# Performance work log

Hardware: AMD Instinct MI355X
Metric: run time of the kernel (lower is better)

The kernel has to match this reference:

```python
import jax, jax.numpy as jnp
import numpy as np

D_MODEL = 1024
N_HEADS = 16
HEAD_DIM = D_MODEL // N_HEADS


def setup_inputs() -> dict:
    key = jax.random.key(0)
    ks = jax.random.split(key, 5)
    T, B = 2048, 2
    x = jax.random.normal(ks[0], (T, B, D_MODEL), dtype=jnp.float32)
    s = 1.0 / np.sqrt(D_MODEL)
    Wq = jax.random.normal(ks[1], (D_MODEL, D_MODEL), dtype=jnp.float32) * s
    Wk = jax.random.normal(ks[2], (D_MODEL, D_MODEL), dtype=jnp.float32) * s
    Wv = jax.random.normal(ks[3], (D_MODEL, D_MODEL), dtype=jnp.float32) * s
    Wo = jax.random.normal(ks[4], (D_MODEL, D_MODEL), dtype=jnp.float32) * s
    return {"x": x, "Wq": Wq, "Wk": Wk, "Wv": Wv, "Wo": Wo}


def reference(x, Wq, Wk, Wv, Wo):
    T, B, C = x.shape
    H, D = N_HEADS, HEAD_DIM

    def split_heads(t):
        # (T,B,C) -> (B,H,T,D), matching view+permute(1,2,0,3)
        return t.reshape(T, B, H, D).transpose(1, 2, 0, 3)

    q = split_heads(x @ Wq.T)
    k = split_heads(x @ Wk.T)
    v = split_heads(x @ Wv.T)

    scale = 1.0 / jnp.sqrt(jnp.asarray(D, dtype=x.dtype))
    scores = jnp.einsum('bhqd,bhkd->bhqk', q, k) * scale  # (B,H,T,T)
    causal = jnp.tril(jnp.ones((T, T), dtype=bool))
    scores = jnp.where(causal, scores, jnp.asarray(-jnp.inf, dtype=scores.dtype))
    probs = jax.nn.softmax(scores, axis=-1)
    ctx = jnp.einsum('bhqk,bhkd->bhqd', probs, v)  # (B,H,T,D)
    ctx = ctx.transpose(2, 0, 1, 3).reshape(T, B, C)
    return ctx @ Wo.T
```

## Files before the change

### kernel.cpp

```cpp
#include <hip/hip_runtime.h>
#include <hip/hip_bf16.h>

#define TT 2048
#define BB 2
#define CC 1024
#define HH 16
#define DD 64
#define MM (TT * BB)

typedef short bf16x8 __attribute__((ext_vector_type(8)));
typedef float f32x4  __attribute__((ext_vector_type(4)));

__device__ inline ushort f2b(float f) {
    union { float f; unsigned u; } v; v.f = f;
    unsigned r = v.u + 0x7FFFu + ((v.u >> 16) & 1u);
    return (ushort)(r >> 16);
}

__device__ inline unsigned pack_bf16(float a, float b) {
    __hip_bfloat162 h = __float22bfloat162_rn(make_float2(a, b));
    union { __hip_bfloat162 h; unsigned u; } c; c.h = h;
    return c.u;
}

__device__ inline void gload_lds16(const ushort* g, ushort* l) {
    __builtin_amdgcn_global_load_lds(
        (const __attribute__((address_space(1))) void*)g,
        (__attribute__((address_space(3))) void*)l, 16, 0, 0);
}

#define XQUADS (MM * CC / 4)
#define WQUADS (CC * CC / 4)
__global__ __launch_bounds__(256) void conv_all(const float* __restrict__ x,
                                                const float* __restrict__ Wq,
                                                const float* __restrict__ Wk,
                                                const float* __restrict__ Wv,
                                                const float* __restrict__ Wo,
                                                ushort* __restrict__ dst) {
    int idx = blockIdx.x * 256 + threadIdx.x;
    const float* src;
    int off;
    if (idx < XQUADS) {
        src = x; off = idx;
    } else {
        int wi = (idx - XQUADS) >> 18;
        off = (idx - XQUADS) & (WQUADS - 1);
        src = (wi == 0) ? Wq : (wi == 1) ? Wk : (wi == 2) ? Wv : Wo;
    }
    float4 v = ((const float4*)src)[off];
    ushort4 o = {f2b(v.x), f2b(v.y), f2b(v.z), f2b(v.w)};
    ((ushort4*)dst)[idx] = o;
}

__global__ __launch_bounds__(256) void gemm_qkv(const ushort* __restrict__ A,
                                                const ushort* __restrict__ B0,
                                                const ushort* __restrict__ B1,
                                                const ushort* __restrict__ B2,
                                                ushort* __restrict__ Oq,
                                                ushort* __restrict__ Ok,
                                                ushort* __restrict__ Ov) {
    __shared__ __align__(16) ushort As[128 * 32];
    __shared__ __align__(16) ushort Bs[128 * 32];

    const int tid = threadIdx.x;
    const int wave = tid >> 6, lane = tid & 63;
    const int quad = lane >> 4, l16 = lane & 15;
    const int wm = wave >> 1, wn = wave & 1;

    const int bm = blockIdx.x * 128;
    const int by = blockIdx.y;
    const int wsel = by >> 3;
    const ushort* Bp = (wsel == 0) ? B0 : (wsel == 1) ? B1 : B2;
    const int bn = (by & 7) * 128;

    const int srow = lane >> 2;
    const int scol = (lane & 3) * 8;

    f32x4 acc[4][4];
#pragma unroll
    for (int i = 0; i < 4; i++)
#pragma unroll
        for (int j = 0; j < 4; j++) acc[i][j] = (f32x4){0.f, 0.f, 0.f, 0.f};

    for (int k0 = 0; k0 < CC; k0 += 32) {
#pragma unroll
        for (int i = 0; i < 2; i++) {
            const int rbase = wave * 32 + i * 16;
            gload_lds16(A + (size_t)(bm + rbase + srow) * CC + k0 + scol,
                        As + rbase * 32);
            gload_lds16(Bp + (size_t)(bn + rbase + srow) * CC + k0 + scol,
                        Bs + rbase * 32);
        }
        __syncthreads();

        bf16x8 af[4], bf[4];
#pragma unroll
        for (int mi = 0; mi < 4; mi++)
            af[mi] = *(const bf16x8*)(As + (wm * 64 + mi * 16 + l16) * 32 + quad * 8);
#pragma unroll
        for (int ni = 0; ni < 4; ni++)
            bf[ni] = *(const bf16x8*)(Bs + (wn * 64 + ni * 16 + l16) * 32 + quad * 8);
#pragma unroll
        for (int mi = 0; mi < 4; mi++)
#pragma unroll
            for (int ni = 0; ni < 4; ni++)
                acc[mi][ni] = __builtin_amdgcn_mfma_f32_16x16x32_bf16(
                    af[mi], bf[ni], acc[mi][ni], 0, 0, 0);
        __syncthreads();
    }

#pragma unroll
    for (int mi = 0; mi < 4; mi++) {
#pragma unroll
        for (int r = 0; r < 4; r++) {
            const int m = bm + wm * 64 + mi * 16 + quad * 4 + r;
#pragma unroll
            for (int ni = 0; ni < 4; ni++) {
                const int colg = bn + wn * 64 + ni * 16 + l16;
                float v = acc[mi][ni][r];
                if (wsel == 0) v *= 0.18033688f;
                const int t = m >> 1, b = m & 1;
                const int h = colg >> 6, d = colg & 63;
                ushort* dst = (wsel == 0) ? Oq : (wsel == 1) ? Ok : Ov;
                dst[(((size_t)(b * HH + h)) * TT + t) * DD + d] = f2b(v);
            }
        }
    }
}

__global__ __launch_bounds__(256) void gemm_out(const ushort* __restrict__ A,
                                                const ushort* __restrict__ Bm,
                                                float* __restrict__ Of) {
    __shared__ __align__(16) ushort As[128 * 32];
    __shared__ __align__(16) ushort Bs[64 * 32];

    const int tid = threadIdx.x;
    const int wave = tid >> 6, lane = tid & 63;
    const int quad = lane >> 4, l16 = lane & 15;

    const int bm = blockIdx.x * 128;
    const int bn = blockIdx.y * 64;

    const int srow = lane >> 2;
    const int scol = (lane & 3) * 8;

    f32x4 acc[2][4];
#pragma unroll
    for (int i = 0; i < 2; i++)
#pragma unroll
        for (int j = 0; j < 4; j++) acc[i][j] = (f32x4){0.f, 0.f, 0.f, 0.f};

    for (int k0 = 0; k0 < CC; k0 += 32) {
#pragma unroll
        for (int i = 0; i < 2; i++) {
            const int rbase = wave * 32 + i * 16;
            gload_lds16(A + (size_t)(bm + rbase + srow) * CC + k0 + scol,
                        As + rbase * 32);
        }
        gload_lds16(Bm + (size_t)(bn + wave * 16 + srow) * CC + k0 + scol,
                    Bs + wave * 16 * 32);
        __syncthreads();

        bf16x8 af[2], bf[4];
#pragma unroll
        for (int mi = 0; mi < 2; mi++)
            af[mi] = *(const bf16x8*)(As + (wave * 32 + mi * 16 + l16) * 32 + quad * 8);
#pragma unroll
        for (int ni = 0; ni < 4; ni++)
            bf[ni] = *(const bf16x8*)(Bs + (ni * 16 + l16) * 32 + quad * 8);
#pragma unroll
        for (int mi = 0; mi < 2; mi++)
#pragma unroll
            for (int ni = 0; ni < 4; ni++)
                acc[mi][ni] = __builtin_amdgcn_mfma_f32_16x16x32_bf16(
                    af[mi], bf[ni], acc[mi][ni], 0, 0, 0);
        __syncthreads();
    }

#pragma unroll
    for (int mi = 0; mi < 2; mi++)
#pragma unroll
        for (int r = 0; r < 4; r++) {
            const int m = bm + wave * 32 + mi * 16 + quad * 4 + r;
#pragma unroll
            for (int ni = 0; ni < 4; ni++)
                Of[(size_t)m * CC + bn + ni * 16 + l16] = acc[mi][ni][r];
        }
}

__global__ __launch_bounds__(256) void prep_kv(const ushort* __restrict__ Kb,
                                               const ushort* __restrict__ Vb,
                                               ushort* __restrict__ Kf,
                                               ushort* __restrict__ Vf) {
    __shared__ __align__(16) ushort Ls[64 * 72];
    const int tile = blockIdx.x;
    const int bh   = blockIdx.y;
    const int t    = threadIdx.x;
    const size_t src = (size_t)bh * TT * DD + (size_t)tile * 64 * DD;
    const size_t dst = (size_t)bh * TT * DD + (size_t)tile * 4096;

#pragma unroll
    for (int i = 0; i < 2; i++) {
        int e = t + i * 256;
        int r = e >> 3, kc = (e & 7) * 8;
        *(uint4*)(Ls + r * 72 + kc) = *(const uint4*)(Kb + src + r * 64 + kc);
    }
    __syncthreads();
#pragma unroll
    for (int i = 0; i < 2; i++) {
        int o = t + i * 256;
        int c = o >> 8, nb = (o >> 6) & 3, lane = o & 63;
        int quad = lane >> 4, l16 = lane & 15;
        int j = nb * 16 + l16, k0 = c * 32 + quad * 8;
        *(uint4*)(Kf + dst + (size_t)o * 8) = *(const uint4*)(Ls + j * 72 + k0);
    }
    __syncthreads();

#pragma unroll
    for (int i = 0; i < 2; i++) {
        int e = t + i * 256;
        int r = e >> 3, kc = (e & 7) * 8;
        *(uint4*)(Ls + r * 72 + kc) = *(const uint4*)(Vb + src + r * 64 + kc);
    }
    __syncthreads();
#pragma unroll
    for (int i = 0; i < 2; i++) {
        int o = t + i * 256;
        int c = o >> 8, db = (o >> 6) & 3, lane = o & 63;
        int quad = lane >> 4, l16 = lane & 15;
        int d = db * 16 + l16;
        ushort tmp[8];
#pragma unroll
        for (int u = 0; u < 8; u++) {
            int jp = c * 32 + quad * 8 + u;
            int j = (jp & 3) * 16 + (jp >> 2);
            tmp[u] = Ls[j * 72 + d];
        }
        *(uint4*)(Vf + dst + (size_t)o * 8) = *(uint4*)tmp;
    }
}

template <bool DIAG>
__device__ __forceinline__ void attn_step(const bf16x8* qa, f32x4* O, float* l,
                                          const bf16x8* kf, const bf16x8* vf,
                                          ushort* P, int j0, int qbase,
                                          int quad, int l16) {
    f32x4 S[4];
#pragma unroll
    for (int nb = 0; nb < 4; nb++) S[nb] = (f32x4){0.f, 0.f, 0.f, 0.f};
#pragma unroll
    for (int c = 0; c < 2; c++)
#pragma unroll
        for (int nb = 0; nb < 4; nb++)
            S[nb] = __builtin_amdgcn_mfma_f32_16x16x32_bf16(qa[c], kf[c * 4 + nb],
                                                            S[nb], 0, 0, 0);

#pragma unroll
    for (int r = 0; r < 4; r++) {
        const int qg = qbase + quad * 4 + r;
        float p[4];
#pragma unroll
        for (int nb = 0; nb < 4; nb++) {
            float s = S[nb][r];
            if (DIAG) { if (j0 + nb * 16 + l16 > qg) s = -1e30f; }
            p[nb] = __builtin_amdgcn_exp2f(s);
        }
        l[r] += (p[0] + p[1]) + (p[2] + p[3]);
        uint2 w; w.x = pack_bf16(p[0], p[1]); w.y = pack_bf16(p[2], p[3]);
        *(uint2*)(P + (quad * 4 + r) * 72 + l16 * 4) = w;
    }

#pragma unroll
    for (int c = 0; c < 2; c++) {
        bf16x8 pa = *(const bf16x8*)(P + l16 * 72 + c * 32 + quad * 8);
#pragma unroll
        for (int db = 0; db < 4; db++)
            O[db] = __builtin_amdgcn_mfma_f32_16x16x32_bf16(pa, vf[c * 4 + db],
                                                            O[db], 0, 0, 0);
    }
}

__global__ __launch_bounds__(256, 2) void attn_mfma(const ushort* __restrict__ Qb,
                                                    const ushort* __restrict__ Kf,
                                                    const ushort* __restrict__ Vf,
                                                    ushort* __restrict__ ctx) {
    __shared__ __align__(16) ushort PsA[4 * 16 * 72];
    __shared__ __align__(16) ushort PsB[4 * 16 * 72];

    const int tid  = threadIdx.x;
    const int wave = tid >> 6;
    const int lane = tid & 63;
    const int quad = lane >> 4;
    const int l16  = lane & 15;

    const int bidx = blockIdx.x;
    const int xcd  = bidx & 7;
    const int slot = bidx >> 3;
    const int bh   = xcd * 4 + (slot >> 4);
    const int p    = slot & 15;

    const int qtA = p, qtB = (TT / 64 - 1) - p;
    const int q0A = qtA * 64 + wave * 16;
    const int q0B = qtB * 64 + wave * 16;

    const size_t baseQK = (size_t)bh * TT * DD;

    bf16x8 qaA[2], qaB[2];
    {
        const ushort* qp = Qb + baseQK + (size_t)(q0A + l16) * DD + quad * 8;
        qaA[0] = *(const bf16x8*)(qp);
        qaA[1] = *(const bf16x8*)(qp + 32);
        const ushort* qp2 = Qb + baseQK + (size_t)(q0B + l16) * DD + quad * 8;
        qaB[0] = *(const bf16x8*)(qp2);
        qaB[1] = *(const bf16x8*)(qp2 + 32);
    }

    f32x4 OA[4], OB[4];
#pragma unroll
    for (int i = 0; i < 4; i++) {
        OA[i] = (f32x4){0.f, 0.f, 0.f, 0.f};
        OB[i] = (f32x4){0.f, 0.f, 0.f, 0.f};
    }
    float lA[4] = {0.f, 0.f, 0.f, 0.f};
    float lB[4] = {0.f, 0.f, 0.f, 0.f};

    ushort* PA = PsA + wave * 16 * 72;
    ushort* PB = PsB + wave * 16 * 72;

    const ushort* Kfp = Kf + baseQK;
    const ushort* Vfp = Vf + baseQK;

    for (int kt = 0; kt <= qtB; kt++) {
        const int j0 = kt * 64;

        bf16x8 kf[8], vf[8];
#pragma unroll
        for (int i = 0; i < 8; i++) {
            kf[i] = *(const bf16x8*)(Kfp + (i << 9) + lane * 8);
            vf[i] = *(const bf16x8*)(Vfp + (i << 9) + lane * 8);
        }

        if (kt == qtB)
            attn_step<true >(qaB, OB, lB, kf, vf, PB, j0, q0B, quad, l16);
        else
            attn_step<false>(qaB, OB, lB, kf, vf, PB, j0, q0B, quad, l16);

        if (kt < qtA)
            attn_step<false>(qaA, OA, lA, kf, vf, PA, j0, q0A, quad, l16);
        else if (kt == qtA)
            attn_step<true >(qaA, OA, lA, kf, vf, PA, j0, q0A, quad, l16);

        Kfp += 4096;
        Vfp += 4096;
    }

    const int b = bh >> 4, h = bh & 15;
#pragma unroll
    for (int r = 0; r < 4; r++) {
        float la = lA[r], lb = lB[r];
        la += __shfl_xor(la, 1); la += __shfl_xor(la, 2);
        la += __shfl_xor(la, 4); la += __shfl_xor(la, 8);
        lb += __shfl_xor(lb, 1); lb += __shfl_xor(lb, 2);
        lb += __shfl_xor(lb, 4); lb += __shfl_xor(lb, 8);
        const float invA = 1.f / la;
        const float invB = 1.f / lb;
        const int tA = q0A + quad * 4 + r;
        const int tB = q0B + quad * 4 + r;
#pragma unroll
        for (int db = 0; db < 4; db++) {
            ctx[((size_t)tA * BB + b) * CC + h * DD + db * 16 + l16] =
                f2b(OA[db][r] * invA);
            ctx[((size_t)tB * BB + b) * CC + h * DD + db * 16 + l16] =
                f2b(OB[db][r] * invB);
        }
    }
}

extern "C" void kernel_launch(void* const* d_in, const int* in_sizes, int n_in,
                              void* d_out, int out_size, void* d_ws, size_t ws_size,
                              hipStream_t stream) {
    const float* x  = (const float*)d_in[0];
    const float* Wq = (const float*)d_in[1];
    const float* Wk = (const float*)d_in[2];
    const float* Wv = (const float*)d_in[3];
    const float* Wo = (const float*)d_in[4];
    float* out = (float*)d_out;

    ushort* xb  = (ushort*)d_ws;
    ushort* Wb  = xb + (size_t)MM * CC;
    ushort* Wqb = Wb;
    ushort* Wkb = Wb + (size_t)CC * CC;
    ushort* Wvb = Wb + 2 * (size_t)CC * CC;
    ushort* Wob = Wb + 3 * (size_t)CC * CC;
    ushort* Qb  = Wb + 4 * (size_t)CC * CC;
    ushort* Kb  = Qb + (size_t)MM * CC;
    ushort* Vb  = Kb + (size_t)MM * CC;
    ushort* Kf  = Vb + (size_t)MM * CC;
    ushort* Vf  = Kf + (size_t)MM * CC;
    ushort* Ctxb = Vf + (size_t)MM * CC;

    conv_all<<<dim3((XQUADS + 4 * WQUADS) / 256), 256, 0, stream>>>(
        x, Wq, Wk, Wv, Wo, xb);

    gemm_qkv<<<dim3(MM / 128, 24), 256, 0, stream>>>(
        xb, Wqb, Wkb, Wvb, Qb, Kb, Vb);

    prep_kv<<<dim3(TT / 64, BB * HH), 256, 0, stream>>>(Kb, Vb, Kf, Vf);

    attn_mfma<<<dim3(512), 256, 0, stream>>>(Qb, Kf, Vf, Ctxb);

    gemm_out<<<dim3(MM / 128, CC / 64), 256, 0, stream>>>(Ctxb, Wob, out);
}
```

Before: 176.5 us.

## Process 32 query rows per wave in attention to reuse K/V fragments

Each wave now handles two 16-row query sub-tiles (32 rows) per key tile, so every K/V fragment loaded from global memory feeds twice as many MFMAs. Query tiles grow to 128 rows and the grid is halved to 256 blocks. Causal end indices are computed per half-block of waves. The trade-off is higher register use (launch bounds drop to 1 block per CU) and fewer blocks, which lowers parallelism and occupancy on a 256-CU part.

```diff
diff --git a/kernel.cpp b/kernel.cpp
--- a/kernel.cpp
+++ b/kernel.cpp
@@ -241,51 +241,61 @@
 }
 
 template <bool DIAG>
-__device__ __forceinline__ void attn_step(const bf16x8* qa, f32x4* O, float* l,
-                                          const bf16x8* kf, const bf16x8* vf,
-                                          ushort* P, int j0, int qbase,
-                                          int quad, int l16) {
-    f32x4 S[4];
-#pragma unroll
-    for (int nb = 0; nb < 4; nb++) S[nb] = (f32x4){0.f, 0.f, 0.f, 0.f};
+__device__ __forceinline__ void attn_step32(const bf16x8* qa,
+                                            f32x4* O,
+                                            float* l,
+                                            const bf16x8* kf, const bf16x8* vf,
+                                            ushort* P, int j0, int qbase,
+                                            int quad, int l16) {
+    f32x4 S[2][4];
+#pragma unroll
+    for (int m = 0; m < 2; m++)
+#pragma unroll
+        for (int nb = 0; nb < 4; nb++) S[m][nb] = (f32x4){0.f, 0.f, 0.f, 0.f};
 #pragma unroll
     for (int c = 0; c < 2; c++)
 #pragma unroll
         for (int nb = 0; nb < 4; nb++)
-            S[nb] = __builtin_amdgcn_mfma_f32_16x16x32_bf16(qa[c], kf[c * 4 + nb],
-                                                            S[nb], 0, 0, 0);
-
-#pragma unroll
-    for (int r = 0; r < 4; r++) {
-        const int qg = qbase + quad * 4 + r;
-        float p[4];
-#pragma unroll
-        for (int nb = 0; nb < 4; nb++) {
-            float s = S[nb][r];
-            if (DIAG) { if (j0 + nb * 16 + l16 > qg) s = -1e30f; }
-            p[nb] = __builtin_amdgcn_exp2f(s);
-        }
-        l[r] += (p[0] + p[1]) + (p[2] + p[3]);
-        uint2 w; w.x = pack_bf16(p[0], p[1]); w.y = pack_bf16(p[2], p[3]);
-        *(uint2*)(P + (quad * 4 + r) * 72 + l16 * 4) = w;
-    }
-
-#pragma unroll
-    for (int c = 0; c < 2; c++) {
-        bf16x8 pa = *(const bf16x8*)(P + l16 * 72 + c * 32 + quad * 8);
-#pragma unroll
-        for (int db = 0; db < 4; db++)
-            O[db] = __builtin_amdgcn_mfma_f32_16x16x32_bf16(pa, vf[c * 4 + db],
-                                                            O[db], 0, 0, 0);
-    }
-}
-
-__global__ __launch_bounds__(256, 2) void attn_mfma(const ushort* __restrict__ Qb,
+#pragma unroll
+            for (int m = 0; m < 2; m++)
+                S[m][nb] = __builtin_amdgcn_mfma_f32_16x16x32_bf16(
+                    qa[m * 2 + c], kf[c * 4 + nb], S[m][nb], 0, 0, 0);
+
+#pragma unroll
+    for (int m = 0; m < 2; m++)
+#pragma unroll
+        for (int r = 0; r < 4; r++) {
+            const int qg = qbase + m * 16 + quad * 4 + r;
+            float p[4];
+#pragma unroll
+            for (int nb = 0; nb < 4; nb++) {
+                float s = S[m][nb][r];
+                if (DIAG) { if (j0 + nb * 16 + l16 > qg) s = -1e30f; }
+                p[nb] = __builtin_amdgcn_exp2f(s);
+            }
+            l[m * 4 + r] += (p[0] + p[1]) + (p[2] + p[3]);
+            uint2 w; w.x = pack_bf16(p[0], p[1]); w.y = pack_bf16(p[2], p[3]);
+            *(uint2*)(P + (m * 16 + quad * 4 + r) * 72 + l16 * 4) = w;
+        }
+
+#pragma unroll
+    for (int m = 0; m < 2; m++)
+#pragma unroll
+        for (int c = 0; c < 2; c++) {
+            bf16x8 pa = *(const bf16x8*)(P + (m * 16 + l16) * 72 + c * 32 + quad * 8);
+#pragma unroll
+            for (int db = 0; db < 4; db++)
+                O[m * 4 + db] = __builtin_amdgcn_mfma_f32_16x16x32_bf16(
+                    pa, vf[c * 4 + db], O[m * 4 + db], 0, 0, 0);
+        }
+}
+
+__global__ __launch_bounds__(256, 1) void attn_mfma(const ushort* __restrict__ Qb,
                                                     const ushort* __restrict__ Kf,
                                                     const ushort* __restrict__ Vf,
                                                     ushort* __restrict__ ctx) {
-    __shared__ __align__(16) ushort PsA[4 * 16 * 72];
-    __shared__ __align__(16) ushort PsB[4 * 16 * 72];
+    __shared__ __align__(16) ushort PsA[4 * 32 * 72];
+    __shared__ __align__(16) ushort PsB[4 * 32 * 72];
 
     const int tid  = threadIdx.x;
     const int wave = tid >> 6;
@@ -296,43 +306,46 @@
     const int bidx = blockIdx.x;
     const int xcd  = bidx & 7;
     const int slot = bidx >> 3;
-    const int bh   = xcd * 4 + (slot >> 4);
-    const int p    = slot & 15;
-
-    const int qtA = p, qtB = (TT / 64 - 1) - p;
-    const int q0A = qtA * 64 + wave * 16;
-    const int q0B = qtB * 64 + wave * 16;
+    const int bh   = xcd * 4 + (slot >> 3);
+    const int p    = slot & 7;
+
+    const int qtA = p, qtB = 15 - p;
+    const int q0A = qtA * 128 + wave * 32;
+    const int q0B = qtB * 128 + wave * 32;
 
     const size_t baseQK = (size_t)bh * TT * DD;
 
-    bf16x8 qaA[2], qaB[2];
-    {
-        const ushort* qp = Qb + baseQK + (size_t)(q0A + l16) * DD + quad * 8;
-        qaA[0] = *(const bf16x8*)(qp);
-        qaA[1] = *(const bf16x8*)(qp + 32);
-        const ushort* qp2 = Qb + baseQK + (size_t)(q0B + l16) * DD + quad * 8;
-        qaB[0] = *(const bf16x8*)(qp2);
-        qaB[1] = *(const bf16x8*)(qp2 + 32);
-    }
-
-    f32x4 OA[4], OB[4];
-#pragma unroll
-    for (int i = 0; i < 4; i++) {
+    bf16x8 qaA[4], qaB[4];
+#pragma unroll
+    for (int m = 0; m < 2; m++) {
+        const ushort* qp = Qb + baseQK + (size_t)(q0A + m * 16 + l16) * DD + quad * 8;
+        qaA[m * 2 + 0] = *(const bf16x8*)(qp);
+        qaA[m * 2 + 1] = *(const bf16x8*)(qp + 32);
+        const ushort* qp2 = Qb + baseQK + (size_t)(q0B + m * 16 + l16) * DD + quad * 8;
+        qaB[m * 2 + 0] = *(const bf16x8*)(qp2);
+        qaB[m * 2 + 1] = *(const bf16x8*)(qp2 + 32);
+    }
+
+    f32x4 OA[8], OB[8];
+#pragma unroll
+    for (int i = 0; i < 8; i++) {
         OA[i] = (f32x4){0.f, 0.f, 0.f, 0.f};
         OB[i] = (f32x4){0.f, 0.f, 0.f, 0.f};
     }
-    float lA[4] = {0.f, 0.f, 0.f, 0.f};
-    float lB[4] = {0.f, 0.f, 0.f, 0.f};
-
-    ushort* PA = PsA + wave * 16 * 72;
-    ushort* PB = PsB + wave * 16 * 72;
+    float lA[8] = {0.f, 0.f, 0.f, 0.f, 0.f, 0.f, 0.f, 0.f};
+    float lB[8] = {0.f, 0.f, 0.f, 0.f, 0.f, 0.f, 0.f, 0.f};
+
+    ushort* PA = PsA + wave * 32 * 72;
+    ushort* PB = PsB + wave * 32 * 72;
+
+    const int hw = wave >> 1;
+    const int ktA_end = 2 * qtA + hw;
+    const int ktB_end = 2 * qtB + hw;
 
     const ushort* Kfp = Kf + baseQK;
     const ushort* Vfp = Vf + baseQK;
 
-    for (int kt = 0; kt <= qtB; kt++) {
-        const int j0 = kt * 64;
-
+    for (int kt = 0; kt <= ktB_end; kt++) {
         bf16x8 kf[8], vf[8];
 #pragma unroll
         for (int i = 0; i < 8; i++) {
@@ -340,15 +353,16 @@
             vf[i] = *(const bf16x8*)(Vfp + (i << 9) + lane * 8);
         }
 
-        if (kt == qtB)
-            attn_step<true >(qaB, OB, lB, kf, vf, PB, j0, q0B, quad, l16);
+        const int j0 = kt * 64;
+        if (kt == ktB_end)
+            attn_step32<true >(qaB, OB, lB, kf, vf, PB, j0, q0B, quad, l16);
         else
-            attn_step<false>(qaB, OB, lB, kf, vf, PB, j0, q0B, quad, l16);
-
-        if (kt < qtA)
-            attn_step<false>(qaA, OA, lA, kf, vf, PA, j0, q0A, quad, l16);
-        else if (kt == qtA)
-            attn_step<true >(qaA, OA, lA, kf, vf, PA, j0, q0A, quad, l16);
+            attn_step32<false>(qaB, OB, lB, kf, vf, PB, j0, q0B, quad, l16);
+
+        if (kt < ktA_end)
+            attn_step32<false>(qaA, OA, lA, kf, vf, PA, j0, q0A, quad, l16);
+        else if (kt == ktA_end)
+            attn_step32<true >(qaA, OA, lA, kf, vf, PA, j0, q0A, quad, l16);
 
         Kfp += 4096;
         Vfp += 4096;
@@ -356,24 +370,26 @@
 
     const int b = bh >> 4, h = bh & 15;
 #pragma unroll
-    for (int r = 0; r < 4; r++) {
-        float la = lA[r], lb = lB[r];
-        la += __shfl_xor(la, 1); la += __shfl_xor(la, 2);
-        la += __shfl_xor(la, 4); la += __shfl_xor(la, 8);
-        lb += __shfl_xor(lb, 1); lb += __shfl_xor(lb, 2);
-        lb += __shfl_xor(lb, 4); lb += __shfl_xor(lb, 8);
-        const float invA = 1.f / la;
-        const float invB = 1.f / lb;
-        const int tA = q0A + quad * 4 + r;
-        const int tB = q0B + quad * 4 + r;
-#pragma unroll
-        for (int db = 0; db < 4; db++) {
-            ctx[((size_t)tA * BB + b) * CC + h * DD + db * 16 + l16] =
-                f2b(OA[db][r] * invA);
-            ctx[((size_t)tB * BB + b) * CC + h * DD + db * 16 + l16] =
-                f2b(OB[db][r] * invB);
-        }
-    }
+    for (int m = 0; m < 2; m++)
+#pragma unroll
+        for (int r = 0; r < 4; r++) {
+            float la = lA[m * 4 + r], lb = lB[m * 4 + r];
+            la += __shfl_xor(la, 1); la += __shfl_xor(la, 2);
+            la += __shfl_xor(la, 4); la += __shfl_xor(la, 8);
+            lb += __shfl_xor(lb, 1); lb += __shfl_xor(lb, 2);
+            lb += __shfl_xor(lb, 4); lb += __shfl_xor(lb, 8);
+            const float invA = 1.f / la;
+            const float invB = 1.f / lb;
+            const int tA = q0A + m * 16 + quad * 4 + r;
+            const int tB = q0B + m * 16 + quad * 4 + r;
+#pragma unroll
+            for (int db = 0; db < 4; db++) {
+                ctx[((size_t)tA * BB + b) * CC + h * DD + db * 16 + l16] =
+                    f2b(OA[m * 4 + db][r] * invA);
+                ctx[((size_t)tB * BB + b) * CC + h * DD + db * 16 + l16] =
+                    f2b(OB[m * 4 + db][r] * invB);
+            }
+        }
 }
 
 extern "C" void kernel_launch(void* const* d_in, const int* in_sizes, int n_in,
@@ -407,7 +423,7 @@
 
     prep_kv<<<dim3(TT / 64, BB * HH), 256, 0, stream>>>(Kb, Vb, Kf, Vf);
 
-    attn_mfma<<<dim3(512), 256, 0, stream>>>(Qb, Kf, Vf, Ctxb);
+    attn_mfma<<<dim3(256), 256, 0, stream>>>(Qb, Kf, Vf, Ctxb);
 
     gemm_out<<<dim3(MM / 128, CC / 64), 256, 0, stream>>>(Ctxb, Wob, out);
 }
```

Result: no change. 178.3 us (+1.0%).

## Compute transposed scores so P stays in registers, removing LDS round-trip

Applied to the files above, without the earlier changes.

Swaps the MFMA operands so the score tile comes out transposed (keys along rows), which lets each lane pack its exp'd probabilities directly into the bf16x8 A-operand of the PV MFMA. The per-wave LDS buffers for P, the writes into them and the reads back out are removed. The V fragment permutation is changed to match the new key ordering, and the row-sum reduction is reorganised into cross-quad shuffles plus a lane broadcast. This cuts LDS traffic and the associated waits from the inner loop, at the cost of tight coupling between the V layout and the new packing order.

```diff
diff --git a/kernel.cpp b/kernel.cpp
--- a/kernel.cpp
+++ b/kernel.cpp
@@ -232,8 +232,7 @@
         ushort tmp[8];
 #pragma unroll
         for (int u = 0; u < 8; u++) {
-            int jp = c * 32 + quad * 8 + u;
-            int j = (jp & 3) * 16 + (jp >> 2);
+            int j = 16 * ((8 * c + u) >> 2) + 4 * quad + (u & 3);
             tmp[u] = Ls[j * 72 + d];
         }
         *(uint4*)(Vf + dst + (size_t)o * 8) = *(uint4*)tmp;
@@ -241,10 +240,9 @@
 }
 
 template <bool DIAG>
-__device__ __forceinline__ void attn_step(const bf16x8* qa, f32x4* O, float* l,
+__device__ __forceinline__ void attn_step(const bf16x8* qa, f32x4* O, float& l,
                                           const bf16x8* kf, const bf16x8* vf,
-                                          ushort* P, int j0, int qbase,
-                                          int quad, int l16) {
+                                          int j0, int qg, int quad) {
     f32x4 S[4];
 #pragma unroll
     for (int nb = 0; nb < 4; nb++) S[nb] = (f32x4){0.f, 0.f, 0.f, 0.f};
@@ -252,41 +250,42 @@
     for (int c = 0; c < 2; c++)
 #pragma unroll
         for (int nb = 0; nb < 4; nb++)
-            S[nb] = __builtin_amdgcn_mfma_f32_16x16x32_bf16(qa[c], kf[c * 4 + nb],
-                                                            S[nb], 0, 0, 0);
-
-#pragma unroll
-    for (int r = 0; r < 4; r++) {
-        const int qg = qbase + quad * 4 + r;
-        float p[4];
-#pragma unroll
-        for (int nb = 0; nb < 4; nb++) {
+            S[nb] = __builtin_amdgcn_mfma_f32_16x16x32_bf16(kf[c * 4 + nb],
+                                                            qa[c], S[nb], 0, 0, 0);
+
+    float p[4][4];
+#pragma unroll
+    for (int nb = 0; nb < 4; nb++)
+#pragma unroll
+        for (int r = 0; r < 4; r++) {
             float s = S[nb][r];
-            if (DIAG) { if (j0 + nb * 16 + l16 > qg) s = -1e30f; }
-            p[nb] = __builtin_amdgcn_exp2f(s);
-        }
-        l[r] += (p[0] + p[1]) + (p[2] + p[3]);
-        uint2 w; w.x = pack_bf16(p[0], p[1]); w.y = pack_bf16(p[2], p[3]);
-        *(uint2*)(P + (quad * 4 + r) * 72 + l16 * 4) = w;
-    }
-
-#pragma unroll
-    for (int c = 0; c < 2; c++) {
-        bf16x8 pa = *(const bf16x8*)(P + l16 * 72 + c * 32 + quad * 8);
-#pragma unroll
-        for (int db = 0; db < 4; db++)
-            O[db] = __builtin_amdgcn_mfma_f32_16x16x32_bf16(pa, vf[c * 4 + db],
-                                                            O[db], 0, 0, 0);
-    }
+            if (DIAG) { if (j0 + nb * 16 + quad * 4 + r > qg) s = -1e30f; }
+            p[nb][r] = __builtin_amdgcn_exp2f(s);
+        }
+#pragma unroll
+    for (int nb = 0; nb < 4; nb++)
+        l += (p[nb][0] + p[nb][1]) + (p[nb][2] + p[nb][3]);
+
+    union { unsigned w[4]; bf16x8 v; } pa0, pa1;
+#pragma unroll
+    for (int w = 0; w < 4; w++) {
+        const int nb = w >> 1;
+        const int rb = (w & 1) * 2;
+        pa0.w[w] = pack_bf16(p[nb][rb], p[nb][rb + 1]);
+        pa1.w[w] = pack_bf16(p[2 + nb][rb], p[2 + nb][rb + 1]);
+    }
+#pragma unroll
+    for (int db = 0; db < 4; db++)
+        O[db] = __builtin_amdgcn_mfma_f32_16x16x32_bf16(pa0.v, vf[db], O[db], 0, 0, 0);
+#pragma unroll
+    for (int db = 0; db < 4; db++)
+        O[db] = __builtin_amdgcn_mfma_f32_16x16x32_bf16(pa1.v, vf[4 + db], O[db], 0, 0, 0);
 }
 
 __global__ __launch_bounds__(256, 2) void attn_mfma(const ushort* __restrict__ Qb,
                                                     const ushort* __restrict__ Kf,
                                                     const ushort* __restrict__ Vf,
                                                     ushort* __restrict__ ctx) {
-    __shared__ __align__(16) ushort PsA[4 * 16 * 72];
-    __shared__ __align__(16) ushort PsB[4 * 16 * 72];
-
     const int tid  = threadIdx.x;
     const int wave = tid >> 6;
     const int lane = tid & 63;
@@ -302,6 +301,8 @@
     const int qtA = p, qtB = (TT / 64 - 1) - p;
     const int q0A = qtA * 64 + wave * 16;
     const int q0B = qtB * 64 + wave * 16;
+    const int qgA = q0A + l16;
+    const int qgB = q0B + l16;
 
     const size_t baseQK = (size_t)bh * TT * DD;
 
@@ -321,11 +322,7 @@
         OA[i] = (f32x4){0.f, 0.f, 0.f, 0.f};
         OB[i] = (f32x4){0.f, 0.f, 0.f, 0.f};
     }
-    float lA[4] = {0.f, 0.f, 0.f, 0.f};
-    float lB[4] = {0.f, 0.f, 0.f, 0.f};
-
-    ushort* PA = PsA + wave * 16 * 72;
-    ushort* PB = PsB + wave * 16 * 72;
+    float lA = 0.f, lB = 0.f;
 
     const ushort* Kfp = Kf + baseQK;
     const ushort* Vfp = Vf + baseQK;
@@ -341,29 +338,27 @@
         }
 
         if (kt == qtB)
-            attn_step<true >(qaB, OB, lB, kf, vf, PB, j0, q0B, quad, l16);
+            attn_step<true >(qaB, OB, lB, kf, vf, j0, qgB, quad);
         else
-            attn_step<false>(qaB, OB, lB, kf, vf, PB, j0, q0B, quad, l16);
+            attn_step<false>(qaB, OB, lB, kf, vf, j0, qgB, quad);
 
         if (kt < qtA)
-            attn_step<false>(qaA, OA, lA, kf, vf, PA, j0, q0A, quad, l16);
+            attn_step<false>(qaA, OA, lA, kf, vf, j0, qgA, quad);
         else if (kt == qtA)
-            attn_step<true >(qaA, OA, lA, kf, vf, PA, j0, q0A, quad, l16);
+            attn_step<true >(qaA, OA, lA, kf, vf, j0, qgA, quad);
 
         Kfp += 4096;
         Vfp += 4096;
     }
 
+    lA += __shfl_xor(lA, 16); lA += __shfl_xor(lA, 32);
+    lB += __shfl_xor(lB, 16); lB += __shfl_xor(lB, 32);
+
     const int b = bh >> 4, h = bh & 15;
 #pragma unroll
     for (int r = 0; r < 4; r++) {
-        float la = lA[r], lb = lB[r];
-        la += __shfl_xor(la, 1); la += __shfl_xor(la, 2);
-        la += __shfl_xor(la, 4); la += __shfl_xor(la, 8);
-        lb += __shfl_xor(lb, 1); lb += __shfl_xor(lb, 2);
-        lb += __shfl_xor(lb, 4); lb += __shfl_xor(lb, 8);
-        const float invA = 1.f / la;
-        const float invB = 1.f / lb;
+        const float invA = 1.f / __shfl(lA, quad * 4 + r);
+        const float invB = 1.f / __shfl(lB, quad * 4 + r);
         const int tA = q0A + quad * 4 + r;
         const int tB = q0B + quad * 4 + r;
 #pragma unroll
```

New measurement: 178.4 us. Within noise of the previous version (+1.1%).
